# Optimization experiments

Measured on AMD Instinct MI355X. Metric: run time of the kernel, lower is better.

Reference implementation:

```python
import jax, jax.numpy as jnp
import numpy as np

N = 50000        # n_nodes
E = 1_600_000    # n_edges (before self-loops)
D_IN, HID, HEADS, D_OUT = 32, 64, 4, 32
NEG_SLOPE = 0.2  # PyG GATConv default leaky_relu slope


def setup_inputs() -> dict:
    key = jax.random.key(0)
    ks = jax.random.split(key, 10)
    x = jax.random.normal(ks[0], (N, D_IN), jnp.float32)
    edge_index = jax.random.randint(ks[1], (2, E), 0, N, dtype=jnp.int64)
    s = 0.1
    W_gcn = jax.random.normal(ks[2], (D_IN, HID), jnp.float32) * s
    b_gcn = jnp.zeros((HID,), jnp.float32)
    W_gat = jax.random.normal(ks[3], (HID, HEADS * HID), jnp.float32) * s
    att_src = jax.random.normal(ks[4], (HEADS, HID), jnp.float32) * s
    att_dst = jax.random.normal(ks[5], (HEADS, HID), jnp.float32) * s
    b_gat = jnp.zeros((HEADS * HID,), jnp.float32)
    W_fc = jax.random.normal(ks[6], (HEADS * HID, D_OUT), jnp.float32) * s
    b_fc = jnp.zeros((D_OUT,), jnp.float32)
    return dict(x=x, edge_index=edge_index, W_gcn=W_gcn, b_gcn=b_gcn,
                W_gat=W_gat, att_src=att_src, att_dst=att_dst, b_gat=b_gat,
                W_fc=W_fc, b_fc=b_fc)


def _add_self_loops(edge_index, n):
    loop = jnp.arange(n, dtype=edge_index.dtype)
    src = jnp.concatenate([edge_index[0], loop])
    dst = jnp.concatenate([edge_index[1], loop])
    return src, dst


def _gcn(x, src, dst, W, b):
    h = x @ W                                               # (N, HID)
    deg = jax.ops.segment_sum(jnp.ones_like(src, jnp.float32), dst, N)
    dinv = jnp.where(deg > 0, jax.lax.rsqrt(deg), 0.0)
    norm = dinv[src] * dinv[dst]                            # (E+N,)
    out = jax.ops.segment_sum(h[src] * norm[:, None], dst, N)
    return out + b


def _gat(x, src, dst, W, att_src, att_dst, b):
    h = (x @ W).reshape(N, HEADS, HID)                      # (N, H, C)
    a_s = jnp.einsum('nhc,hc->nh', h, att_src)              # (N, H)
    a_d = jnp.einsum('nhc,hc->nh', h, att_dst)
    e = jax.nn.leaky_relu(a_s[src] + a_d[dst], NEG_SLOPE)   # (E+N, H)
    # softmax over incoming edges per destination node
    m = jax.ops.segment_max(e, dst, N)                      # every dst has a self-loop
    w = jnp.exp(e - m[dst])
    denom = jax.ops.segment_sum(w, dst, N)
    alpha = w / denom[dst]                                  # (E+N, H)
    out = jax.ops.segment_sum(h[src] * alpha[:, :, None], dst, N)
    return out.reshape(N, HEADS * HID) + b


def reference(x, edge_index, W_gcn, b_gcn, W_gat, att_src, att_dst, b_gat, W_fc, b_fc):
    src, dst = _add_self_loops(edge_index, N)
    h = jax.nn.relu(_gcn(x, src, dst, W_gcn, b_gcn))        # dropout: eval mode (identity)
    h = jax.nn.relu(_gat(h, src, dst, W_gat, att_src, att_dst, b_gat))
    return h @ W_fc + b_fc
```

## Files before the change

kernel.cpp:

```cpp
#include <hip/hip_runtime.h>
#include <hip/hip_bf16.h>
#include <hip/hip_fp16.h>
#include <math.h>

#define N_NODES 50000
#define N_EDGES 1600000
#define D_IN    32
#define HID     64
#define HEADS   4
#define D_OUT   32
#define NEG_SLOPE 0.2f
#define NTILES 3125

#define CQG 64
#define CQA 32

#define NBKT 196
#define NBLK_A 391
#define TILE_A 4096
#define GH (NBKT * NBLK_A)
#define NSB 300
#define CAP 10240

typedef _Float16 half8 __attribute__((ext_vector_type(8)));
typedef float    f32x4 __attribute__((ext_vector_type(4)));
typedef float    f32x2 __attribute__((ext_vector_type(2)));

__global__ __launch_bounds__(256) void histA(const int* __restrict__ edge,
                                             int* __restrict__ ghist) {
    __shared__ int hist[4][NBKT];
    int t = threadIdx.x, wv = t >> 6;
    for (int i = t; i < 4 * NBKT; i += 256) ((int*)hist)[i] = 0;
    __syncthreads();
    int base = blockIdx.x * TILE_A;
#pragma unroll
    for (int k = 0; k < 16; k++) {
        int i = base + k * 256 + t;
        if (i < N_EDGES) atomicAdd(&hist[wv][edge[N_EDGES + i] >> 8], 1);
    }
    __syncthreads();
    for (int b = t; b < NBKT; b += 256)
        ghist[b * NBLK_A + blockIdx.x] = hist[0][b] + hist[1][b] + hist[2][b] + hist[3][b];
}

__global__ __launch_bounds__(256) void scanB1(const int* __restrict__ g,
                                              int* __restrict__ bsum) {
    int t = threadIdx.x;
    int i = blockIdx.x * 256 + t;
    int v = (i < GH) ? g[i] : 0;
#pragma unroll
    for (int off = 32; off; off >>= 1) v += __shfl_xor(v, off);
    __shared__ int ws[4];
    if ((t & 63) == 0) ws[t >> 6] = v;
    __syncthreads();
    if (t == 0) bsum[blockIdx.x] = ws[0] + ws[1] + ws[2] + ws[3];
}

__global__ __launch_bounds__(320) void scanB2_attvec(int* __restrict__ bsum,
                                                     const float* __restrict__ W,
                                                     const float* __restrict__ att_s,
                                                     const float* __restrict__ att_d,
                                                     float* __restrict__ vsrc,
                                                     float* __restrict__ vdst) {
    int t = threadIdx.x, lane = t & 63, wv = t >> 6;
    if (blockIdx.x == 0) {
        int v = (t < NSB) ? bsum[t] : 0;
        int inc = v;
#pragma unroll
        for (int d = 1; d < 64; d <<= 1) {
            int u = __shfl_up(inc, d);
            if (lane >= d) inc += u;
        }
        __shared__ int ws[5];
        if (lane == 63) ws[wv] = inc;
        __syncthreads();
        int add = 0;
#pragma unroll
        for (int j = 0; j < 5; j++) if (j < wv) add += ws[j];
        if (t < NSB) bsum[t] = add + inc - v;
    } else if (t < 256) {
        int h = t >> 6, k = t & 63;
        float s_ = 0.f, d_ = 0.f;
#pragma unroll 8
        for (int c = 0; c < 64; c++) {
            float w = W[k * 256 + h * 64 + c];
            s_ += w * att_s[h * 64 + c];
            d_ += w * att_d[h * 64 + c];
        }
        vsrc[h * 64 + k] = s_;
        vdst[h * 64 + k] = d_;
    }
}

__global__ __launch_bounds__(256) void scanB3(int* __restrict__ g,
                                              const int* __restrict__ bsum) {
    int t = threadIdx.x, lane = t & 63, wv = t >> 6;
    int i = blockIdx.x * 256 + t;
    int v = (i < GH) ? g[i] : 0;
    int inc = v;
#pragma unroll
    for (int d = 1; d < 64; d <<= 1) {
        int u = __shfl_up(inc, d);
        if (lane >= d) inc += u;
    }
    __shared__ int ws[4];
    if (lane == 63) ws[wv] = inc;
    __syncthreads();
    int add = 0;
#pragma unroll
    for (int j = 0; j < 4; j++) if (j < wv) add += ws[j];
    if (i < GH) g[i] = bsum[blockIdx.x] + add + inc - v;
}

__global__ __launch_bounds__(256) void scatterC(const int* __restrict__ edge,
                                                const int* __restrict__ ghist,
                                                unsigned* __restrict__ tmp) {
    __shared__ int cur[NBKT];
    int t = threadIdx.x;
    if (t < NBKT) cur[t] = ghist[t * NBLK_A + blockIdx.x];
    __syncthreads();
    int base = blockIdx.x * TILE_A;
#pragma unroll
    for (int k = 0; k < 16; k++) {
        int i = base + k * 256 + t;
        if (i < N_EDGES) {
            int s = edge[i], d = edge[N_EDGES + i];
            int pos = atomicAdd(&cur[d >> 8], 1);
            tmp[pos] = ((unsigned)d << 16) | (unsigned)s;
        }
    }
}

__global__ __launch_bounds__(256) void sortD(const unsigned* __restrict__ tmp,
                                             const int* __restrict__ ghist,
                                             unsigned short* __restrict__ colidx,
                                             int* __restrict__ rowptr,
                                             float* __restrict__ dinv) {
    __shared__ unsigned char  dl8[CAP];
    __shared__ unsigned short s16[CAP];
    __shared__ unsigned short o16[CAP];
    __shared__ int hist[4][256];
    __shared__ int excl[256];
    __shared__ int wsum[4];
    int t = threadIdx.x, lane = t & 63, wv = t >> 6;
    int b = blockIdx.x;
    int lo = ghist[b * NBLK_A];
    int hi = (b < NBKT - 1) ? ghist[(b + 1) * NBLK_A] : N_EDGES;
    int size = hi - lo;
    if (size > CAP) size = CAP;
    for (int i = t; i < 4 * 256; i += 256) ((int*)hist)[i] = 0;
    __syncthreads();
    for (int i = t; i < size; i += 256) {
        unsigned key = tmp[lo + i];
        int dl = (key >> 16) & 255;
        dl8[i] = (unsigned char)dl;
        s16[i] = (unsigned short)(key & 0xFFFF);
        atomicAdd(&hist[wv][dl], 1);
    }
    __syncthreads();
    int h = hist[0][t] + hist[1][t] + hist[2][t] + hist[3][t];
    int inc = h;
#pragma unroll
    for (int d = 1; d < 64; d <<= 1) {
        int u = __shfl_up(inc, d);
        if (lane >= d) inc += u;
    }
    if (lane == 63) wsum[wv] = inc;
    __syncthreads();
    int add = 0;
#pragma unroll
    for (int j = 0; j < 4; j++) if (j < wv) add += wsum[j];
    int ex = inc - h + add;
    excl[t] = ex;
    int node = b * 256 + t;
    if (node < N_NODES) {
        rowptr[node] = lo + ex;
        dinv[node]   = rsqrtf((float)(h + 1));
    }
    if (b == NBKT - 1 && t == 0) rowptr[N_NODES] = N_EDGES;
    __syncthreads();
    for (int i = t; i < size; i += 256) {
        int pos = atomicAdd(&excl[dl8[i]], 1);
        o16[pos] = s16[i];
    }
    __syncthreads();
    for (int i = t; i < size; i += 256) colidx[lo + i] = o16[i];
}

__global__ __launch_bounds__(256) void gemm1(const float* __restrict__ x,
                                             const float* __restrict__ W,
                                             const float* __restrict__ dinv,
                                             __half* __restrict__ h,
                                             __half* __restrict__ h1) {
    __shared__ float Wl[D_IN * HID];
    int t = threadIdx.x;
    if (blockIdx.x == 0 && t < HID) {
        h [(size_t)N_NODES * HID + t] = __float2half(0.f);
        h1[(size_t)N_NODES * HID + t] = __float2half(0.f);
    }
    for (int i = t; i < D_IN * HID; i += 256) Wl[i] = W[i];
    __syncthreads();
    int c = t & 63, rw = t >> 6;
    int r0 = blockIdx.x * 32;
#pragma unroll
    for (int rr = 0; rr < 8; rr++) {
        int r = r0 + rr * 4 + rw;
        if (r >= N_NODES) break;
        const float4* xr4 = (const float4*)(x + r * D_IN);
        float acc = 0.f;
#pragma unroll
        for (int k4 = 0; k4 < D_IN / 4; k4++) {
            float4 xv = xr4[k4];
            int k = k4 * 4;
            acc += xv.x * Wl[(k+0)*HID + c] + xv.y * Wl[(k+1)*HID + c]
                 + xv.z * Wl[(k+2)*HID + c] + xv.w * Wl[(k+3)*HID + c];
        }
        h[r * HID + c] = __float2half(acc * dinv[r]);
    }
}

__global__ __launch_bounds__(256) void gcn_agg(const __half* __restrict__ h,
                                               const int* __restrict__ rowptr,
                                               const unsigned short* __restrict__ colidx,
                                               const float* __restrict__ dinv,
                                               const float* __restrict__ b,
                                               const float* __restrict__ vsrc,
                                               const float* __restrict__ vdst,
                                               __half* __restrict__ h1,
                                               float* __restrict__ as_o,
                                               float* __restrict__ ad_o) {
    __shared__ int sbuf[4][8][CQG + 1];
    int lane = threadIdx.x & 63, wv = threadIdx.x >> 6;
    int oct = lane >> 3, ol = lane & 7;
    int n = blockIdx.x * 32 + wv * 8 + oct;
    int nn = min(n, N_NODES - 1);
    int rp = rowptr[nn], re = rowptr[nn + 1];
    int deg = (n < N_NODES) ? (re - rp) : 0;
    int dm = deg;
    dm = max(dm, __shfl_xor(dm, 8));
    dm = max(dm, __shfl_xor(dm, 16));
    dm = max(dm, __shfl_xor(dm, 32));
    f32x4 a0 = {0.f,0.f,0.f,0.f}, a1 = {0.f,0.f,0.f,0.f};
    const __half* hp = h + ol * 8;
    int* sq = sbuf[wv][oct];
    for (int cb = 0; cb < dm; cb += CQG) {
        int m  = min(CQG, max(deg - cb, 0));
        int mm = min(CQG, dm - cb);
        int mm8 = (mm + 7) & ~7;
        for (int j = ol; j < m; j += 8)
            sq[j] = (int)colidx[rp + cb + j] * HID;
        for (int j = m + ol; j < mm8; j += 8)
            sq[j] = N_NODES * HID;
        for (int i0 = 0; i0 < mm8; i0 += 8) {
            float4 raw[8];
#pragma unroll
            for (int k = 0; k < 8; k++)
                raw[k] = *(const float4*)(hp + sq[i0 + k]);
#pragma unroll
            for (int k = 0; k < 8; k++) {
                __half2 g0 = __builtin_bit_cast(__half2, raw[k].x);
                __half2 g1 = __builtin_bit_cast(__half2, raw[k].y);
                __half2 g2 = __builtin_bit_cast(__half2, raw[k].z);
                __half2 g3 = __builtin_bit_cast(__half2, raw[k].w);
                float2 f0 = __half22float2(g0), f1 = __half22float2(g1);
                float2 f2 = __half22float2(g2), f3 = __half22float2(g3);
                a0.x += f0.x; a0.y += f0.y; a0.z += f1.x; a0.w += f1.y;
                a1.x += f2.x; a1.y += f2.y; a1.z += f3.x; a1.w += f3.y;
            }
        }
    }
    {
        float4 raw = *(const float4*)(hp + nn * HID);
        __half2 g0 = __builtin_bit_cast(__half2, raw.x);
        __half2 g1 = __builtin_bit_cast(__half2, raw.y);
        __half2 g2 = __builtin_bit_cast(__half2, raw.z);
        __half2 g3 = __builtin_bit_cast(__half2, raw.w);
        float2 f0 = __half22float2(g0), f1 = __half22float2(g1);
        float2 f2 = __half22float2(g2), f3 = __half22float2(g3);
        a0.x += f0.x; a0.y += f0.y; a0.z += f1.x; a0.w += f1.y;
        a1.x += f2.x; a1.y += f2.y; a1.z += f3.x; a1.w += f3.y;
    }
    float dn = dinv[nn];
    const float4 bb0 = *(const float4*)&b[ol * 8];
    const float4 bb1 = *(const float4*)&b[ol * 8 + 4];
    float v0 = fmaxf(a0.x * dn + bb0.x, 0.f);
    float v1 = fmaxf(a0.y * dn + bb0.y, 0.f);
    float v2 = fmaxf(a0.z * dn + bb0.z, 0.f);
    float v3 = fmaxf(a0.w * dn + bb0.w, 0.f);
    float v4 = fmaxf(a1.x * dn + bb1.x, 0.f);
    float v5 = fmaxf(a1.y * dn + bb1.y, 0.f);
    float v6 = fmaxf(a1.z * dn + bb1.z, 0.f);
    float v7 = fmaxf(a1.w * dn + bb1.w, 0.f);
    if (n < N_NODES) {
        __half2 p0 = __floats2half2_rn(v0, v1);
        __half2 p1 = __floats2half2_rn(v2, v3);
        __half2 p2 = __floats2half2_rn(v4, v5);
        __half2 p3 = __floats2half2_rn(v6, v7);
        float4 pk;
        pk.x = __builtin_bit_cast(float, p0);
        pk.y = __builtin_bit_cast(float, p1);
        pk.z = __builtin_bit_cast(float, p2);
        pk.w = __builtin_bit_cast(float, p3);
        *(float4*)&h1[n * HID + ol * 8] = pk;
    }
#pragma unroll
    for (int hh = 0; hh < 4; hh++) {
        const float4 s0 = *(const float4*)&vsrc[hh * 64 + ol * 8];
        const float4 s1 = *(const float4*)&vsrc[hh * 64 + ol * 8 + 4];
        const float4 d0 = *(const float4*)&vdst[hh * 64 + ol * 8];
        const float4 d1 = *(const float4*)&vdst[hh * 64 + ol * 8 + 4];
        float vs = v0*s0.x + v1*s0.y + v2*s0.z + v3*s0.w
                 + v4*s1.x + v5*s1.y + v6*s1.z + v7*s1.w;
        float vd = v0*d0.x + v1*d0.y + v2*d0.z + v3*d0.w
                 + v4*d1.x + v5*d1.y + v6*d1.z + v7*d1.w;
#pragma unroll
        for (int off = 4; off > 0; off >>= 1) {
            vs += __shfl_xor(vs, off);
            vd += __shfl_xor(vd, off);
        }
        if (ol == 0 && n < N_NODES) {
            as_o[n * 4 + hh] = vs;
            ad_o[n * 4 + hh] = vd;
        }
    }
}

__global__ __launch_bounds__(256) void gat_agg(const __half* __restrict__ h1,
                                               const int* __restrict__ rowptr,
                                               const unsigned short* __restrict__ colidx,
                                               const float* __restrict__ a_s,
                                               const float* __restrict__ a_d,
                                               __half* __restrict__ u) {
    __shared__ float4 wbuf[4][8][CQA + 1];
    __shared__ int    sbuf[4][8][CQA + 1];
    int lane = threadIdx.x & 63, wv = threadIdx.x >> 6;
    int oct = lane >> 3, ol = lane & 7;
    int n = blockIdx.x * 32 + wv * 8 + oct;
    int nn = min(n, N_NODES - 1);
    int rp = rowptr[nn], re = rowptr[nn + 1];
    int deg = (n < N_NODES) ? (re - rp) : 0;
    int dm = deg;
    dm = max(dm, __shfl_xor(dm, 8));
    dm = max(dm, __shfl_xor(dm, 16));
    dm = max(dm, __shfl_xor(dm, 32));
    float4 ad4 = *(const float4*)&a_d[nn * 4];

    float dnx = 0.f, dny = 0.f, dnz = 0.f, dnw = 0.f;
    f32x4 accA[4], accB[4];
#pragma unroll
    for (int hh = 0; hh < 4; hh++) { accA[hh] = (f32x4){0.f,0.f,0.f,0.f}; accB[hh] = (f32x4){0.f,0.f,0.f,0.f}; }
    const __half* hp = h1 + ol * 8;
    int*    sq = sbuf[wv][oct];
    float4* wq = wbuf[wv][oct];
    for (int cb = 0; cb < dm; cb += CQA) {
        int m  = min(CQA, max(deg - cb, 0));
        int mm = min(CQA, dm - cb);
        int mm8 = (mm + 7) & ~7;
        for (int j = ol; j < m; j += 8) {
            int s = colidx[rp + cb + j];
            float4 a = *(const float4*)&a_s[s * 4];
            float vx = a.x + ad4.x; vx = fmaxf(vx, NEG_SLOPE * vx);
            float vy = a.y + ad4.y; vy = fmaxf(vy, NEG_SLOPE * vy);
            float vz = a.z + ad4.z; vz = fmaxf(vz, NEG_SLOPE * vz);
            float vw = a.w + ad4.w; vw = fmaxf(vw, NEG_SLOPE * vw);
            float wx = __expf(vx), wy = __expf(vy);
            float wz = __expf(vz), ww = __expf(vw);
            dnx += wx; dny += wy; dnz += wz; dnw += ww;
            sq[j] = s * HID;
            wq[j] = make_float4(wx, wy, wz, ww);
        }
        for (int j = m + ol; j < mm8; j += 8) {
            sq[j] = N_NODES * HID;
            wq[j] = make_float4(0.f, 0.f, 0.f, 0.f);
        }
        for (int i0 = 0; i0 < mm8; i0 += 8) {
            float4 raw[8];
#pragma unroll
            for (int k = 0; k < 8; k++)
                raw[k] = *(const float4*)(hp + sq[i0 + k]);
#pragma unroll
            for (int k = 0; k < 8; k++) {
                float4 w4 = wq[i0 + k];
                __half2 g0 = __builtin_bit_cast(__half2, raw[k].x);
                __half2 g1 = __builtin_bit_cast(__half2, raw[k].y);
                __half2 g2 = __builtin_bit_cast(__half2, raw[k].z);
                __half2 g3 = __builtin_bit_cast(__half2, raw[k].w);
                float2 f0 = __half22float2(g0), f1 = __half22float2(g1);
                float2 f2 = __half22float2(g2), f3 = __half22float2(g3);
                f32x4 flo = {f0.x, f0.y, f1.x, f1.y};
                f32x4 fhi = {f2.x, f2.y, f3.x, f3.y};
                f32x4 wxv = {w4.x, w4.x, w4.x, w4.x};
                f32x4 wyv = {w4.y, w4.y, w4.y, w4.y};
                f32x4 wzv = {w4.z, w4.z, w4.z, w4.z};
                f32x4 wwv = {w4.w, w4.w, w4.w, w4.w};
                accA[0] += wxv * flo; accB[0] += wxv * fhi;
                accA[1] += wyv * flo; accB[1] += wyv * fhi;
                accA[2] += wzv * flo; accB[2] += wzv * fhi;
                accA[3] += wwv * flo; accB[3] += wwv * fhi;
            }
        }
    }
#pragma unroll
    for (int off = 4; off > 0; off >>= 1) {
        dnx += __shfl_xor(dnx, off);
        dny += __shfl_xor(dny, off);
        dnz += __shfl_xor(dnz, off);
        dnw += __shfl_xor(dnw, off);
    }
    float4 asn = *(const float4*)&a_s[nn * 4];
    float sx = asn.x + ad4.x; sx = fmaxf(sx, NEG_SLOPE * sx);
    float sy = asn.y + ad4.y; sy = fmaxf(sy, NEG_SLOPE * sy);
    float sz = asn.z + ad4.z; sz = fmaxf(sz, NEG_SLOPE * sz);
    float sw = asn.w + ad4.w; sw = fmaxf(sw, NEG_SLOPE * sw);
    float wsx = __expf(sx), wsy = __expf(sy);
    float wsz = __expf(sz), wsw = __expf(sw);
    dnx += wsx; dny += wsy; dnz += wsz; dnw += wsw;
    {
        float4 raw = *(const float4*)(hp + nn * HID);
        __half2 g0 = __builtin_bit_cast(__half2, raw.x);
        __half2 g1 = __builtin_bit_cast(__half2, raw.y);
        __half2 g2 = __builtin_bit_cast(__half2, raw.z);
        __half2 g3 = __builtin_bit_cast(__half2, raw.w);
        float2 f0 = __half22float2(g0), f1 = __half22float2(g1);
        float2 f2 = __half22float2(g2), f3 = __half22float2(g3);
        f32x4 flo = {f0.x, f0.y, f1.x, f1.y};
        f32x4 fhi = {f2.x, f2.y, f3.x, f3.y};
        accA[0] += (f32x4){wsx,wsx,wsx,wsx} * flo; accB[0] += (f32x4){wsx,wsx,wsx,wsx} * fhi;
        accA[1] += (f32x4){wsy,wsy,wsy,wsy} * flo; accB[1] += (f32x4){wsy,wsy,wsy,wsy} * fhi;
        accA[2] += (f32x4){wsz,wsz,wsz,wsz} * flo; accB[2] += (f32x4){wsz,wsz,wsz,wsz} * fhi;
        accA[3] += (f32x4){wsw,wsw,wsw,wsw} * flo; accB[3] += (f32x4){wsw,wsw,wsw,wsw} * fhi;
    }
    if (n < N_NODES) {
        float r4[4] = {1.f / dnx, 1.f / dny, 1.f / dnz, 1.f / dnw};
        __half* up = u + (size_t)n * 256 + ol * 8;
#pragma unroll
        for (int hh = 0; hh < 4; hh++) {
            float r = r4[hh];
            __half2 p0 = __floats2half2_rn(accA[hh].x * r, accA[hh].y * r);
            __half2 p1 = __floats2half2_rn(accA[hh].z * r, accA[hh].w * r);
            __half2 p2 = __floats2half2_rn(accB[hh].x * r, accB[hh].y * r);
            __half2 p3 = __floats2half2_rn(accB[hh].z * r, accB[hh].w * r);
            float4 pk;
            pk.x = __builtin_bit_cast(float, p0);
            pk.y = __builtin_bit_cast(float, p1);
            pk.z = __builtin_bit_cast(float, p2);
            pk.w = __builtin_bit_cast(float, p3);
            *(float4*)&up[hh * 64] = pk;
        }
    }
}

__global__ __launch_bounds__(256) void gemm2b(const __half* __restrict__ u,
                                              const float* __restrict__ W,
                                              const float* __restrict__ b,
                                              __half* __restrict__ h2) {
    int lane = threadIdx.x & 63, hd = threadIdx.x >> 6;
    int quad = lane >> 4, l16 = lane & 15;
    half8 Bf[4][2];
#pragma unroll
    for (int nt = 0; nt < 4; nt++)
#pragma unroll
        for (int kc = 0; kc < 2; kc++) {
            const float* wp = W + (kc * 32 + quad * 8) * 256 + hd * 64 + nt * 16 + l16;
#pragma unroll
            for (int j = 0; j < 8; j++)
                Bf[nt][kc][j] = (_Float16)wp[j * 256];
        }
    float bb[4];
#pragma unroll
    for (int nt = 0; nt < 4; nt++) bb[nt] = b[hd * 64 + nt * 16 + l16];

    int rt0 = blockIdx.x * 5;
#pragma unroll
    for (int i = 0; i < 5; i++) {
        int rt = rt0 + i;
        const __half* up = u + ((size_t)(rt * 16 + l16)) * 256 + hd * 64 + quad * 8;
        half8 A0 = *(const half8*)(const void*)up;
        half8 A1 = *(const half8*)(const void*)(up + 32);
        f32x4 acc[4];
#pragma unroll
        for (int nt = 0; nt < 4; nt++) {
            acc[nt] = (f32x4){0.f, 0.f, 0.f, 0.f};
            acc[nt] = __builtin_amdgcn_mfma_f32_16x16x32_f16(A0, Bf[nt][0], acc[nt], 0, 0, 0);
            acc[nt] = __builtin_amdgcn_mfma_f32_16x16x32_f16(A1, Bf[nt][1], acc[nt], 0, 0, 0);
        }
#pragma unroll
        for (int nt = 0; nt < 4; nt++) {
            int col = hd * 64 + nt * 16 + l16;
#pragma unroll
            for (int reg = 0; reg < 4; reg++) {
                int row = rt * 16 + quad * 4 + reg;
                h2[(size_t)row * 256 + col] = __float2half(fmaxf(acc[nt][reg] + bb[nt], 0.f));
            }
        }
    }
}

__global__ __launch_bounds__(256) void gemm3(const __half* __restrict__ h2,
                                             const float* __restrict__ W,
                                             const float* __restrict__ b,
                                             float* __restrict__ out) {
    int lane = threadIdx.x & 63, wv = threadIdx.x >> 6;
    int quad = lane >> 4, l16 = lane & 15;
    half8 Bf[2][8];
#pragma unroll
    for (int nt = 0; nt < 2; nt++)
#pragma unroll
        for (int kc = 0; kc < 8; kc++) {
            const float* wp = W + (kc * 32 + quad * 8) * 32 + nt * 16 + l16;
#pragma unroll
            for (int j = 0; j < 8; j++)
                Bf[nt][kc][j] = (_Float16)wp[j * 32];
        }
    float bb0 = b[l16], bb1 = b[16 + l16];

    for (int tile = blockIdx.x * 4 + wv; tile < NTILES; tile += gridDim.x * 4) {
        const __half* hp = h2 + (size_t)(tile * 16 + l16) * 256 + quad * 8;
        f32x4 acc0 = {0.f, 0.f, 0.f, 0.f};
        f32x4 acc1 = {0.f, 0.f, 0.f, 0.f};
#pragma unroll
        for (int kc = 0; kc < 8; kc++) {
            half8 A = *(const half8*)(const void*)(hp + kc * 32);
            acc0 = __builtin_amdgcn_mfma_f32_16x16x32_f16(A, Bf[0][kc], acc0, 0, 0, 0);
            acc1 = __builtin_amdgcn_mfma_f32_16x16x32_f16(A, Bf[1][kc], acc1, 0, 0, 0);
        }
#pragma unroll
        for (int reg = 0; reg < 4; reg++) {
            int row = tile * 16 + quad * 4 + reg;
            out[row * 32 + l16]      = acc0[reg] + bb0;
            out[row * 32 + 16 + l16] = acc1[reg] + bb1;
        }
    }
}

extern "C" void kernel_launch(void* const* d_in, const int* in_sizes, int n_in,
                              void* d_out, int out_size, void* d_ws, size_t ws_size,
                              hipStream_t stream) {
    const float* x      = (const float*)d_in[0];
    const int*   edge   = (const int*)  d_in[1];
    const float* W_gcn  = (const float*)d_in[2];
    const float* b_gcn  = (const float*)d_in[3];
    const float* W_gat  = (const float*)d_in[4];
    const float* att_s  = (const float*)d_in[5];
    const float* att_d  = (const float*)d_in[6];
    const float* b_gat  = (const float*)d_in[7];
    const float* W_fc   = (const float*)d_in[8];
    const float* b_fc   = (const float*)d_in[9];
    float* out = (float*)d_out;

    char* p = (char*)d_ws;
    auto alloc = [&](size_t bytes) {
        char* q = p;
        p += (bytes + 255) & ~(size_t)255;
        return q;
    };
    __half* h     = (__half*)alloc((size_t)(N_NODES + 1) * HID * 2);
    __half* h1    = (__half*)alloc((size_t)(N_NODES + 1) * HID * 2);
    __half* u     = (__half*)alloc((size_t)N_NODES * 256 * 2);
    __half* h2    = (__half*)alloc((size_t)N_NODES * 256 * 2);
    float* as_a   = (float*)alloc((size_t)N_NODES * 4 * 4);
    float* ad_a   = (float*)alloc((size_t)N_NODES * 4 * 4);
    float* dinv   = (float*)alloc((size_t)N_NODES * 4);
    int*   rowptr = (int*)  alloc((size_t)(N_NODES + 1) * 4);
    unsigned short* colidx = (unsigned short*)alloc((size_t)N_EDGES * 2);
    int*   ghist  = (int*)  alloc((size_t)GH * 4);
    int*   bsum   = (int*)  alloc((size_t)NSB * 4);
    unsigned* tmp = (unsigned*)alloc((size_t)N_EDGES * 4);
    float* vsrc   = (float*)alloc((size_t)HEADS * HID * 4);
    float* vdst   = (float*)alloc((size_t)HEADS * HID * 4);

    histA        <<<NBLK_A, 256, 0, stream>>>(edge, ghist);
    scanB1       <<<NSB, 256, 0, stream>>>(ghist, bsum);
    scanB2_attvec<<<2, 320, 0, stream>>>(bsum, W_gat, att_s, att_d, vsrc, vdst);
    scanB3       <<<NSB, 256, 0, stream>>>(ghist, bsum);
    scatterC     <<<NBLK_A, 256, 0, stream>>>(edge, ghist, tmp);
    sortD        <<<NBKT, 256, 0, stream>>>(tmp, ghist, colidx, rowptr, dinv);

    gemm1   <<<(N_NODES + 31) / 32, 256, 0, stream>>>(x, W_gcn, dinv, h, h1);
    gcn_agg <<<(N_NODES + 31) / 32, 256, 0, stream>>>(h, rowptr, colidx, dinv, b_gcn,
                                                      vsrc, vdst, h1, as_a, ad_a);

    gat_agg <<<(N_NODES + 31) / 32, 256, 0, stream>>>(h1, rowptr, colidx, as_a, ad_a, u);
    gemm2b  <<<625, 256, 0, stream>>>(u, W_gat, b_gat, h2);

    gemm3   <<<256, 256, 0, stream>>>(h2, W_fc, b_fc, out);
}
```

Baseline: 221.9 us.

## Fuse GAT output GEMM and final FC GEMM through shared memory

Merges the gemm2b and gemm3 kernels into one kernel. Each block computes a 64-row tile of relu(u·W_gat+b) into an LDS buffer, then runs the FC projection straight from LDS. This removes the 25.6 MB fp16 h2 round trip through global memory and one kernel launch. In exchange each thread holds more weight registers (both B-fragment sets), which may lower occupancy, and there is a block-wide sync.

```diff
diff --git a/kernel.cpp b/kernel.cpp
--- a/kernel.cpp
+++ b/kernel.cpp
@@ -450,30 +450,45 @@
     }
 }
 
-__global__ __launch_bounds__(256) void gemm2b(const __half* __restrict__ u,
-                                              const float* __restrict__ W,
-                                              const float* __restrict__ b,
-                                              __half* __restrict__ h2) {
+__global__ __launch_bounds__(256) void gemm23(const __half* __restrict__ u,
+                                              const float* __restrict__ Wg,
+                                              const float* __restrict__ bg,
+                                              const float* __restrict__ Wf,
+                                              const float* __restrict__ bf,
+                                              float* __restrict__ out) {
+    __shared__ __half h2s[64][264];
     int lane = threadIdx.x & 63, hd = threadIdx.x >> 6;
     int quad = lane >> 4, l16 = lane & 15;
-    half8 Bf[4][2];
+    half8 Bg[4][2];
 #pragma unroll
     for (int nt = 0; nt < 4; nt++)
 #pragma unroll
         for (int kc = 0; kc < 2; kc++) {
-            const float* wp = W + (kc * 32 + quad * 8) * 256 + hd * 64 + nt * 16 + l16;
+            const float* wp = Wg + (kc * 32 + quad * 8) * 256 + hd * 64 + nt * 16 + l16;
 #pragma unroll
             for (int j = 0; j < 8; j++)
-                Bf[nt][kc][j] = (_Float16)wp[j * 256];
-        }
-    float bb[4];
-#pragma unroll
-    for (int nt = 0; nt < 4; nt++) bb[nt] = b[hd * 64 + nt * 16 + l16];
-
-    int rt0 = blockIdx.x * 5;
-#pragma unroll
-    for (int i = 0; i < 5; i++) {
-        int rt = rt0 + i;
+                Bg[nt][kc][j] = (_Float16)wp[j * 256];
+        }
+    float bbg[4];
+#pragma unroll
+    for (int nt = 0; nt < 4; nt++) bbg[nt] = bg[hd * 64 + nt * 16 + l16];
+    half8 Bf[2][8];
+#pragma unroll
+    for (int nt = 0; nt < 2; nt++)
+#pragma unroll
+        for (int kc = 0; kc < 8; kc++) {
+            const float* wp = Wf + (kc * 32 + quad * 8) * 32 + nt * 16 + l16;
+#pragma unroll
+            for (int j = 0; j < 8; j++)
+                Bf[nt][kc][j] = (_Float16)wp[j * 32];
+        }
+    float bb0 = bf[l16], bb1 = bf[16 + l16];
+
+    int t0 = blockIdx.x * 4;
+#pragma unroll
+    for (int i = 0; i < 4; i++) {
+        int rt = t0 + i;
+        if (rt >= NTILES) break;
         const __half* up = u + ((size_t)(rt * 16 + l16)) * 256 + hd * 64 + quad * 8;
         half8 A0 = *(const half8*)(const void*)up;
         half8 A1 = *(const half8*)(const void*)(up + 32);
@@ -481,52 +496,31 @@
 #pragma unroll
         for (int nt = 0; nt < 4; nt++) {
             acc[nt] = (f32x4){0.f, 0.f, 0.f, 0.f};
-            acc[nt] = __builtin_amdgcn_mfma_f32_16x16x32_f16(A0, Bf[nt][0], acc[nt], 0, 0, 0);
-            acc[nt] = __builtin_amdgcn_mfma_f32_16x16x32_f16(A1, Bf[nt][1], acc[nt], 0, 0, 0);
+            acc[nt] = __builtin_amdgcn_mfma_f32_16x16x32_f16(A0, Bg[nt][0], acc[nt], 0, 0, 0);
+            acc[nt] = __builtin_amdgcn_mfma_f32_16x16x32_f16(A1, Bg[nt][1], acc[nt], 0, 0, 0);
         }
 #pragma unroll
         for (int nt = 0; nt < 4; nt++) {
             int col = hd * 64 + nt * 16 + l16;
 #pragma unroll
-            for (int reg = 0; reg < 4; reg++) {
-                int row = rt * 16 + quad * 4 + reg;
-                h2[(size_t)row * 256 + col] = __float2half(fmaxf(acc[nt][reg] + bb[nt], 0.f));
-            }
-        }
-    }
-}
-
-__global__ __launch_bounds__(256) void gemm3(const __half* __restrict__ h2,
-                                             const float* __restrict__ W,
-                                             const float* __restrict__ b,
-                                             float* __restrict__ out) {
-    int lane = threadIdx.x & 63, wv = threadIdx.x >> 6;
-    int quad = lane >> 4, l16 = lane & 15;
-    half8 Bf[2][8];
-#pragma unroll
-    for (int nt = 0; nt < 2; nt++)
-#pragma unroll
-        for (int kc = 0; kc < 8; kc++) {
-            const float* wp = W + (kc * 32 + quad * 8) * 32 + nt * 16 + l16;
-#pragma unroll
-            for (int j = 0; j < 8; j++)
-                Bf[nt][kc][j] = (_Float16)wp[j * 32];
-        }
-    float bb0 = b[l16], bb1 = b[16 + l16];
-
-    for (int tile = blockIdx.x * 4 + wv; tile < NTILES; tile += gridDim.x * 4) {
-        const __half* hp = h2 + (size_t)(tile * 16 + l16) * 256 + quad * 8;
+            for (int reg = 0; reg < 4; reg++)
+                h2s[i * 16 + quad * 4 + reg][col] = __float2half(fmaxf(acc[nt][reg] + bbg[nt], 0.f));
+        }
+    }
+    __syncthreads();
+    int rt = t0 + hd;
+    if (rt < NTILES) {
         f32x4 acc0 = {0.f, 0.f, 0.f, 0.f};
         f32x4 acc1 = {0.f, 0.f, 0.f, 0.f};
 #pragma unroll
         for (int kc = 0; kc < 8; kc++) {
-            half8 A = *(const half8*)(const void*)(hp + kc * 32);
+            half8 A = *(const half8*)(const void*)&h2s[hd * 16 + l16][kc * 32 + quad * 8];
             acc0 = __builtin_amdgcn_mfma_f32_16x16x32_f16(A, Bf[0][kc], acc0, 0, 0, 0);
             acc1 = __builtin_amdgcn_mfma_f32_16x16x32_f16(A, Bf[1][kc], acc1, 0, 0, 0);
         }
 #pragma unroll
         for (int reg = 0; reg < 4; reg++) {
-            int row = tile * 16 + quad * 4 + reg;
+            int row = rt * 16 + quad * 4 + reg;
             out[row * 32 + l16]      = acc0[reg] + bb0;
             out[row * 32 + 16 + l16] = acc1[reg] + bb1;
         }
@@ -557,7 +551,6 @@
     __half* h     = (__half*)alloc((size_t)(N_NODES + 1) * HID * 2);
     __half* h1    = (__half*)alloc((size_t)(N_NODES + 1) * HID * 2);
     __half* u     = (__half*)alloc((size_t)N_NODES * 256 * 2);
-    __half* h2    = (__half*)alloc((size_t)N_NODES * 256 * 2);
     float* as_a   = (float*)alloc((size_t)N_NODES * 4 * 4);
     float* ad_a   = (float*)alloc((size_t)N_NODES * 4 * 4);
     float* dinv   = (float*)alloc((size_t)N_NODES * 4);
@@ -581,7 +574,6 @@
                                                       vsrc, vdst, h1, as_a, ad_a);
 
     gat_agg <<<(N_NODES + 31) / 32, 256, 0, stream>>>(h1, rowptr, colidx, as_a, ad_a, u);
-    gemm2b  <<<625, 256, 0, stream>>>(u, W_gat, b_gat, h2);
-
-    gemm3   <<<256, 256, 0, stream>>>(h2, W_fc, b_fc, out);
-}
+
+    gemm23  <<<(NTILES + 3) / 4, 256, 0, stream>>>(u, W_gat, b_gat, W_fc, b_fc, out);
+}
```

Measured after the change: 214.5 us. -3.3%, faster.
